# Kernel tuning notes

Measured on AMD Instinct MI355X. Metric: run time of the kernel, lower is better.

## Reference

```python
import jax, jax.numpy as jnp
import numpy as np

MUL_VAL = 4.0

def _fake_quant(v, qmin, qmax):
    # per-tensor float scale from abs-max (brevitas Int8*PerTensorFloat style)
    s = jnp.max(jnp.abs(v)) / 127.0
    q = jnp.clip(jnp.round(v / s), qmin, qmax) * s
    return q

def setup_inputs() -> dict:
    key = jax.random.key(0)
    k1, k2, k3 = jax.random.split(key, 3)
    N, IN, OUT = 8192, 4096, 4096
    x = jax.random.normal(k1, (N, IN), dtype=jnp.float32)
    W = jax.random.normal(k2, (OUT, IN), dtype=jnp.float32) * 0.02
    b = jax.random.normal(k3, (OUT,), dtype=jnp.float32) * 0.01
    return {"x": x, "W": W, "b": b}

def reference(x, W, b):
    # Int8ActPerTensorFloat: signed 8-bit, non-narrow range [-128, 127]
    qx = _fake_quant(x, -128.0, 127.0)
    # Int8WeightPerTensorFloat: signed 8-bit, narrow range [-127, 127]
    qw = _fake_quant(W, -127.0, 127.0)
    y = jnp.einsum('ni,oi->no', qx, qw) + b
    return MUL_VAL * y
```

## Files before the change

kernel.cpp:

```cpp
#include <hip/hip_runtime.h>

typedef int int4v __attribute__((ext_vector_type(4)));
typedef int int16v __attribute__((ext_vector_type(16)));

#define BM 256
#define BN 256
#define BKB 128

__device__ __forceinline__ void async_copy16(const void* g, void* l) {
  __builtin_amdgcn_global_load_lds((const __attribute__((address_space(1))) void*)g,
                                   (__attribute__((address_space(3))) void*)l, 16, 0, 0);
}

__global__ __launch_bounds__(256) void absmax2_kernel(
    const float* __restrict__ x, size_t n4x,
    const float* __restrict__ w, size_t n4w,
    unsigned* __restrict__ out, int xb) {
  const float4* src;
  size_t n4;
  unsigned* dst;
  int bid, nb;
  if ((int)blockIdx.x < xb) {
    src = (const float4*)x; n4 = n4x; dst = out; bid = blockIdx.x; nb = xb;
  } else {
    src = (const float4*)w; n4 = n4w; dst = out + 1; bid = blockIdx.x - xb; nb = gridDim.x - xb;
  }
  size_t i = (size_t)bid * blockDim.x + threadIdx.x;
  size_t stride = (size_t)nb * blockDim.x;
  float m = 0.0f;
  for (; i < n4; i += stride) {
    float4 v = src[i];
    m = fmaxf(m, fmaxf(fmaxf(fabsf(v.x), fabsf(v.y)), fmaxf(fabsf(v.z), fabsf(v.w))));
  }
#pragma unroll
  for (int off = 32; off > 0; off >>= 1)
    m = fmaxf(m, __shfl_down(m, off, 64));
  __shared__ float red[4];
  int wave = threadIdx.x >> 6, lane = threadIdx.x & 63;
  if (lane == 0) red[wave] = m;
  __syncthreads();
  if (threadIdx.x == 0) {
    m = fmaxf(fmaxf(red[0], red[1]), fmaxf(red[2], red[3]));
    atomicMax(dst, __float_as_uint(m));
  }
}

__global__ __launch_bounds__(256) void quant2_kernel(
    const float* __restrict__ x, char* __restrict__ qx, size_t nx,
    const float* __restrict__ w, char* __restrict__ qw, size_t nw,
    const unsigned* __restrict__ amax, int xb) {
  const float* src;
  char* dst;
  size_t n;
  float r, lo;
  int bid, nb;
  if ((int)blockIdx.x < xb) {
    src = x; dst = qx; n = nx; r = 127.0f / __uint_as_float(amax[0]);
    lo = -128.0f; bid = blockIdx.x; nb = xb;
  } else {
    src = w; dst = qw; n = nw; r = 127.0f / __uint_as_float(amax[1]);
    lo = -127.0f; bid = blockIdx.x - xb; nb = gridDim.x - xb;
  }
  size_t i = ((size_t)bid * blockDim.x + threadIdx.x) * 8;
  size_t stride = (size_t)nb * blockDim.x * 8;
  for (; i < n; i += stride) {
    float4 v0 = *(const float4*)(src + i);
    float4 v1 = *(const float4*)(src + i + 4);
    float f[8] = {v0.x, v0.y, v0.z, v0.w, v1.x, v1.y, v1.z, v1.w};
    unsigned w0 = 0, w1 = 0;
#pragma unroll
    for (int j = 0; j < 4; ++j) {
      int q0 = (int)fminf(fmaxf(rintf(f[j] * r), lo), 127.0f);
      int q1 = (int)fminf(fmaxf(rintf(f[4 + j] * r), lo), 127.0f);
      w0 |= (unsigned)(q0 & 0xff) << (8 * j);
      w1 |= (unsigned)(q1 & 0xff) << (8 * j);
    }
    uint2 u; u.x = w0; u.y = w1;
    *(uint2*)(dst + i) = u;
  }
}


#define STAGE_A4(buf_, t_) do {                                                \
    const char* ga_ = gA + (size_t)(t_) * BKB;                                 \
    int r0_ = wave * 8;                                                        \
    async_copy16(ga_ + (size_t)(r0_      ) * K, &As[buf_][(r0_      ) * BKB]); \
    async_copy16(ga_ + (size_t)(r0_ +  64) * K, &As[buf_][(r0_ +  64) * BKB]); \
    async_copy16(ga_ + (size_t)(r0_ + 128) * K, &As[buf_][(r0_ + 128) * BKB]); \
    async_copy16(ga_ + (size_t)(r0_ + 192) * K, &As[buf_][(r0_ + 192) * BKB]); \
  } while (0)

#define STAGE_B4(buf_, t_) do {                                                \
    const char* gb_ = gB + (size_t)(t_) * BKB;                                 \
    int r0_ = wave * 8;                                                        \
    async_copy16(gb_ + (size_t)(r0_      ) * K, &Bs[buf_][(r0_      ) * BKB]); \
    async_copy16(gb_ + (size_t)(r0_ +  64) * K, &Bs[buf_][(r0_ +  64) * BKB]); \
    async_copy16(gb_ + (size_t)(r0_ + 128) * K, &Bs[buf_][(r0_ + 128) * BKB]); \
    async_copy16(gb_ + (size_t)(r0_ + 192) * K, &Bs[buf_][(r0_ + 192) * BKB]); \
  } while (0)

#define VM0 asm volatile("s_waitcnt vmcnt(0)" ::: "memory")
#define VMN ((void)0)
#define NOSTG ((void)0)

#define MFMA32 __builtin_amdgcn_mfma_i32_32x32x32_i8

#define PHASE(bb_, so_, STG, VMW) do {                                         \
    asm volatile("" ::: "memory");                                             \
    const char* Ab_ = &As[bb_][(wr * 128 + r32) * BKB];                        \
    const char* Bb_ = &Bs[bb_][(wc * 64 + r32) * BKB];                         \
    int4v a0_ = *(const int4v*)(Ab_ + 0 * 32 * BKB + (so_));                   \
    int4v a1_ = *(const int4v*)(Ab_ + 1 * 32 * BKB + (so_));                   \
    int4v a2_ = *(const int4v*)(Ab_ + 2 * 32 * BKB + (so_));                   \
    int4v a3_ = *(const int4v*)(Ab_ + 3 * 32 * BKB + (so_));                   \
    int4v b0_ = *(const int4v*)(Bb_ + 0 * 32 * BKB + (so_));                   \
    int4v b1_ = *(const int4v*)(Bb_ + 1 * 32 * BKB + (so_));                   \
    STG;                                                                       \
    __builtin_amdgcn_s_barrier();                                              \
    __builtin_amdgcn_s_setprio(1);                                             \
    acc[0][0] = MFMA32(a0_, b0_, acc[0][0], 0, 0, 0);                          \
    acc[0][1] = MFMA32(a0_, b1_, acc[0][1], 0, 0, 0);                          \
    acc[1][0] = MFMA32(a1_, b0_, acc[1][0], 0, 0, 0);                          \
    acc[1][1] = MFMA32(a1_, b1_, acc[1][1], 0, 0, 0);                          \
    acc[2][0] = MFMA32(a2_, b0_, acc[2][0], 0, 0, 0);                          \
    acc[2][1] = MFMA32(a2_, b1_, acc[2][1], 0, 0, 0);                          \
    acc[3][0] = MFMA32(a3_, b0_, acc[3][0], 0, 0, 0);                          \
    acc[3][1] = MFMA32(a3_, b1_, acc[3][1], 0, 0, 0);                          \
    __builtin_amdgcn_s_setprio(0);                                             \
    VMW;                                                                       \
    asm volatile("" ::: "memory");                                             \
    __builtin_amdgcn_s_barrier();                                              \
  } while (0)

#define TILE(bb_, STG0, STG1, VMW3) do {                                       \
    PHASE(bb_, so0, STG0, VMN);                                                \
    PHASE(bb_, so1, STG1, VMN);                                                \
    PHASE(bb_, so2, NOSTG, VMN);                                               \
    PHASE(bb_, so3, NOSTG, VMW3);                                              \
  } while (0)

__global__ __launch_bounds__(512, 2) void gemm_i8_kernel(
    const char* __restrict__ qx, const char* __restrict__ qw,
    const float* __restrict__ bias, const unsigned* __restrict__ amax,
    float* __restrict__ out, int M, int N, int K) {
  __shared__ __align__(16) char As[2][BM * BKB];
  __shared__ __align__(16) char Bs[2][BN * BKB];
  const int tid = threadIdx.x;
  const int wave = tid >> 6, lane = tid & 63;
  const int wr = wave >> 2, wc = wave & 3;

  int tilesM = M / BM, tilesN = N / BN;
  int T = tilesM * tilesN;
  int p = blockIdx.x;
  int tile;
  if ((T & 7) == 0) tile = (p & 7) * (T >> 3) + (p >> 3);
  else tile = p;
  int bm = (tile % tilesM) * BM;
  int bn = (tile / tilesM) * BN;

  const int grow = lane >> 3;
  const int gcol = ((lane & 7) ^ grow) * 16;
  const char* gA = qx + (size_t)(bm + grow) * K + gcol;
  const char* gB = qw + (size_t)(bn + grow) * K + gcol;

  const int r32 = lane & 31, hi = lane >> 5, l7 = lane & 7;
  const int so0 = ((0 + hi) ^ l7) * 16;
  const int so1 = ((2 + hi) ^ l7) * 16;
  const int so2 = ((4 + hi) ^ l7) * 16;
  const int so3 = ((6 + hi) ^ l7) * 16;

  const int NT = K >> 7;

  int16v acc[4][2] = {};

  STAGE_A4(0, 0);
  STAGE_B4(0, 0);
  VM0;
  __builtin_amdgcn_s_barrier();

  int t = 0;
  for (; t < NT - 2; t += 2) {
    TILE(0, STAGE_A4(1, t + 1), STAGE_B4(1, t + 1), VM0);
    TILE(1, STAGE_A4(0, t + 2), STAGE_B4(0, t + 2), VM0);
  }
  TILE(0, STAGE_A4(1, NT - 1), STAGE_B4(1, NT - 1), VM0);
  TILE(1, NOSTG, NOSTG, VMN);

  float fx = __uint_as_float(amax[0]) * (1.0f / 127.0f);
  float fw = __uint_as_float(amax[1]) * (1.0f / 127.0f);
  float scale = 4.0f * fx * fw;
  int col = lane & 31;
  int rbh = 4 * hi;
#pragma unroll
  for (int n = 0; n < 2; ++n) {
    int gn = bn + wc * 64 + n * 32 + col;
    float b4 = 4.0f * bias[gn];
#pragma unroll
    for (int m = 0; m < 4; ++m) {
      size_t rowb = (size_t)(bm + wr * 128 + m * 32 + rbh);
#pragma unroll
      for (int g = 0; g < 4; ++g)
#pragma unroll
        for (int rr = 0; rr < 4; ++rr)
          __builtin_nontemporal_store(
              scale * (float)acc[m][n][g * 4 + rr] + b4,
              out + (rowb + g * 8 + rr) * N + gn);
    }
  }
}

extern "C" void kernel_launch(void* const* d_in, const int* in_sizes, int n_in,
                              void* d_out, int out_size, void* d_ws, size_t ws_size,
                              hipStream_t stream) {
  const float* x = (const float*)d_in[0];
  const float* W = (const float*)d_in[1];
  const float* b = (const float*)d_in[2];
  float* out = (float*)d_out;

  int Nv = in_sizes[2];
  int K = in_sizes[1] / Nv;
  int M = in_sizes[0] / K;

  size_t nx = (size_t)M * K, nw = (size_t)Nv * K;
  unsigned* amax = (unsigned*)d_ws;
  char* qx = (char*)d_ws + 256;
  char* qw = qx + nx;

  hipMemsetAsync(d_ws, 0, 8, stream);
  absmax2_kernel<<<1536, 256, 0, stream>>>(x, nx / 4, W, nw / 4, amax, 1024);
  quant2_kernel<<<3072, 256, 0, stream>>>(x, qx, nx, W, qw, nw, amax, 2048);
  gemm_i8_kernel<<<(M / BM) * (Nv / BN), 512, 0, stream>>>(qx, qw, b, amax, out, M, Nv, K);
}
```

Baseline: 443.5 us.

## Store GEMM LDS tiles in MFMA fragment order and unroll absmax/quant loops

```diff
diff --git a/kernel.cpp b/kernel.cpp
--- a/kernel.cpp
+++ b/kernel.cpp
@@ -27,11 +27,22 @@
   }
   size_t i = (size_t)bid * blockDim.x + threadIdx.x;
   size_t stride = (size_t)nb * blockDim.x;
-  float m = 0.0f;
+  float m0 = 0.f, m1 = 0.f, m2 = 0.f, m3 = 0.f;
+  for (; i + 3 * stride < n4; i += 4 * stride) {
+    float4 v0 = src[i];
+    float4 v1 = src[i + stride];
+    float4 v2 = src[i + 2 * stride];
+    float4 v3 = src[i + 3 * stride];
+    m0 = fmaxf(m0, fmaxf(fmaxf(fabsf(v0.x), fabsf(v0.y)), fmaxf(fabsf(v0.z), fabsf(v0.w))));
+    m1 = fmaxf(m1, fmaxf(fmaxf(fabsf(v1.x), fabsf(v1.y)), fmaxf(fabsf(v1.z), fabsf(v1.w))));
+    m2 = fmaxf(m2, fmaxf(fmaxf(fabsf(v2.x), fabsf(v2.y)), fmaxf(fabsf(v2.z), fabsf(v2.w))));
+    m3 = fmaxf(m3, fmaxf(fmaxf(fabsf(v3.x), fabsf(v3.y)), fmaxf(fabsf(v3.z), fabsf(v3.w))));
+  }
   for (; i < n4; i += stride) {
     float4 v = src[i];
-    m = fmaxf(m, fmaxf(fmaxf(fabsf(v.x), fabsf(v.y)), fmaxf(fabsf(v.z), fabsf(v.w))));
-  }
+    m0 = fmaxf(m0, fmaxf(fmaxf(fabsf(v.x), fabsf(v.y)), fmaxf(fabsf(v.z), fabsf(v.w))));
+  }
+  float m = fmaxf(fmaxf(m0, m1), fmaxf(m2, m3));
 #pragma unroll
   for (int off = 32; off > 0; off >>= 1)
     m = fmaxf(m, __shfl_down(m, off, 64));
@@ -43,6 +54,24 @@
     m = fmaxf(fmaxf(red[0], red[1]), fmaxf(red[2], red[3]));
     atomicMax(dst, __float_as_uint(m));
   }
+}
+
+__device__ __forceinline__ void quant8(const float* __restrict__ src,
+                                       char* __restrict__ dst, size_t i,
+                                       float r, float lo) {
+  float4 v0 = *(const float4*)(src + i);
+  float4 v1 = *(const float4*)(src + i + 4);
+  float f[8] = {v0.x, v0.y, v0.z, v0.w, v1.x, v1.y, v1.z, v1.w};
+  unsigned w0 = 0, w1 = 0;
+#pragma unroll
+  for (int j = 0; j < 4; ++j) {
+    int q0 = (int)fminf(fmaxf(rintf(f[j] * r), lo), 127.0f);
+    int q1 = (int)fminf(fmaxf(rintf(f[4 + j] * r), lo), 127.0f);
+    w0 |= (unsigned)(q0 & 0xff) << (8 * j);
+    w1 |= (unsigned)(q1 & 0xff) << (8 * j);
+  }
+  uint2 u; u.x = w0; u.y = w1;
+  *(uint2*)(dst + i) = u;
 }
 
 __global__ __launch_bounds__(256) void quant2_kernel(
@@ -63,40 +92,30 @@
   }
   size_t i = ((size_t)bid * blockDim.x + threadIdx.x) * 8;
   size_t stride = (size_t)nb * blockDim.x * 8;
-  for (; i < n; i += stride) {
-    float4 v0 = *(const float4*)(src + i);
-    float4 v1 = *(const float4*)(src + i + 4);
-    float f[8] = {v0.x, v0.y, v0.z, v0.w, v1.x, v1.y, v1.z, v1.w};
-    unsigned w0 = 0, w1 = 0;
-#pragma unroll
-    for (int j = 0; j < 4; ++j) {
-      int q0 = (int)fminf(fmaxf(rintf(f[j] * r), lo), 127.0f);
-      int q1 = (int)fminf(fmaxf(rintf(f[4 + j] * r), lo), 127.0f);
-      w0 |= (unsigned)(q0 & 0xff) << (8 * j);
-      w1 |= (unsigned)(q1 & 0xff) << (8 * j);
-    }
-    uint2 u; u.x = w0; u.y = w1;
-    *(uint2*)(dst + i) = u;
-  }
+  for (; i + stride < n; i += 2 * stride) {
+    quant8(src, dst, i, r, lo);
+    quant8(src, dst, i + stride, r, lo);
+  }
+  if (i < n) quant8(src, dst, i, r, lo);
 }
 
 
 #define STAGE_A4(buf_, t_) do {                                                \
-    const char* ga_ = gA + (size_t)(t_) * BKB;                                 \
-    int r0_ = wave * 8;                                                        \
-    async_copy16(ga_ + (size_t)(r0_      ) * K, &As[buf_][(r0_      ) * BKB]); \
-    async_copy16(ga_ + (size_t)(r0_ +  64) * K, &As[buf_][(r0_ +  64) * BKB]); \
-    async_copy16(ga_ + (size_t)(r0_ + 128) * K, &As[buf_][(r0_ + 128) * BKB]); \
-    async_copy16(ga_ + (size_t)(r0_ + 192) * K, &As[buf_][(r0_ + 192) * BKB]); \
+    const char* ga_ = gA + (size_t)(wave * 32) * K + (size_t)(t_) * BKB;       \
+    char* la_ = &As[buf_][wave * 4096];                                        \
+    async_copy16(ga_ +  0, la_ +    0);                                        \
+    async_copy16(ga_ + 32, la_ + 1024);                                        \
+    async_copy16(ga_ + 64, la_ + 2048);                                        \
+    async_copy16(ga_ + 96, la_ + 3072);                                        \
   } while (0)
 
 #define STAGE_B4(buf_, t_) do {                                                \
-    const char* gb_ = gB + (size_t)(t_) * BKB;                                 \
-    int r0_ = wave * 8;                                                        \
-    async_copy16(gb_ + (size_t)(r0_      ) * K, &Bs[buf_][(r0_      ) * BKB]); \
-    async_copy16(gb_ + (size_t)(r0_ +  64) * K, &Bs[buf_][(r0_ +  64) * BKB]); \
-    async_copy16(gb_ + (size_t)(r0_ + 128) * K, &Bs[buf_][(r0_ + 128) * BKB]); \
-    async_copy16(gb_ + (size_t)(r0_ + 192) * K, &Bs[buf_][(r0_ + 192) * BKB]); \
+    const char* gb_ = gB + (size_t)(wave * 32) * K + (size_t)(t_) * BKB;       \
+    char* lb_ = &Bs[buf_][wave * 4096];                                        \
+    async_copy16(gb_ +  0, lb_ +    0);                                        \
+    async_copy16(gb_ + 32, lb_ + 1024);                                        \
+    async_copy16(gb_ + 64, lb_ + 2048);                                        \
+    async_copy16(gb_ + 96, lb_ + 3072);                                        \
   } while (0)
 
 #define VM0 asm volatile("s_waitcnt vmcnt(0)" ::: "memory")
@@ -105,16 +124,16 @@
 
 #define MFMA32 __builtin_amdgcn_mfma_i32_32x32x32_i8
 
-#define PHASE(bb_, so_, STG, VMW) do {                                         \
+#define PHASE(bb_, ks_, STG, VMW) do {                                         \
     asm volatile("" ::: "memory");                                             \
-    const char* Ab_ = &As[bb_][(wr * 128 + r32) * BKB];                        \
-    const char* Bb_ = &Bs[bb_][(wc * 64 + r32) * BKB];                         \
-    int4v a0_ = *(const int4v*)(Ab_ + 0 * 32 * BKB + (so_));                   \
-    int4v a1_ = *(const int4v*)(Ab_ + 1 * 32 * BKB + (so_));                   \
-    int4v a2_ = *(const int4v*)(Ab_ + 2 * 32 * BKB + (so_));                   \
-    int4v a3_ = *(const int4v*)(Ab_ + 3 * 32 * BKB + (so_));                   \
-    int4v b0_ = *(const int4v*)(Bb_ + 0 * 32 * BKB + (so_));                   \
-    int4v b1_ = *(const int4v*)(Bb_ + 1 * 32 * BKB + (so_));                   \
+    const char* Ab_ = &As[bb_][wr * 16384 + hoff];                             \
+    const char* Bb_ = &Bs[bb_][wc * 8192 + hoff];                              \
+    int4v a0_ = *(const int4v*)(Ab_ + 0 * 4096 + (ks_) * 1024);                \
+    int4v a1_ = *(const int4v*)(Ab_ + 1 * 4096 + (ks_) * 1024);                \
+    int4v a2_ = *(const int4v*)(Ab_ + 2 * 4096 + (ks_) * 1024);                \
+    int4v a3_ = *(const int4v*)(Ab_ + 3 * 4096 + (ks_) * 1024);                \
+    int4v b0_ = *(const int4v*)(Bb_ + 0 * 4096 + (ks_) * 1024);                \
+    int4v b1_ = *(const int4v*)(Bb_ + 1 * 4096 + (ks_) * 1024);                \
     STG;                                                                       \
     __builtin_amdgcn_s_barrier();                                              \
     __builtin_amdgcn_s_setprio(1);                                             \
@@ -133,10 +152,10 @@
   } while (0)
 
 #define TILE(bb_, STG0, STG1, VMW3) do {                                       \
-    PHASE(bb_, so0, STG0, VMN);                                                \
-    PHASE(bb_, so1, STG1, VMN);                                                \
-    PHASE(bb_, so2, NOSTG, VMN);                                               \
-    PHASE(bb_, so3, NOSTG, VMW3);                                              \
+    PHASE(bb_, 0, STG0, VMN);                                                  \
+    PHASE(bb_, 1, STG1, VMN);                                                  \
+    PHASE(bb_, 2, NOSTG, VMN);                                                 \
+    PHASE(bb_, 3, NOSTG, VMW3);                                                \
   } while (0)
 
 __global__ __launch_bounds__(512, 2) void gemm_i8_kernel(
@@ -158,16 +177,10 @@
   int bm = (tile % tilesM) * BM;
   int bn = (tile / tilesM) * BN;
 
-  const int grow = lane >> 3;
-  const int gcol = ((lane & 7) ^ grow) * 16;
-  const char* gA = qx + (size_t)(bm + grow) * K + gcol;
-  const char* gB = qw + (size_t)(bn + grow) * K + gcol;
-
-  const int r32 = lane & 31, hi = lane >> 5, l7 = lane & 7;
-  const int so0 = ((0 + hi) ^ l7) * 16;
-  const int so1 = ((2 + hi) ^ l7) * 16;
-  const int so2 = ((4 + hi) ^ l7) * 16;
-  const int so3 = ((6 + hi) ^ l7) * 16;
+  const char* gA = qx + (size_t)(bm + (lane & 31)) * K + (lane >> 5) * 16;
+  const char* gB = qw + (size_t)(bn + (lane & 31)) * K + (lane >> 5) * 16;
+
+  const int hoff = (lane >> 5) * 512 + (lane & 31) * 16;
 
   const int NT = K >> 7;
 
@@ -190,7 +203,7 @@
   float fw = __uint_as_float(amax[1]) * (1.0f / 127.0f);
   float scale = 4.0f * fx * fw;
   int col = lane & 31;
-  int rbh = 4 * hi;
+  int rbh = 4 * (lane >> 5);
 #pragma unroll
   for (int n = 0; n < 2; ++n) {
     int gn = bn + wc * 64 + n * 32 + col;
```

Result: slower. 510.9 us (+15.2%).
